# Performance work log

Hardware: AMD Instinct MI355X
Metric: run time of the kernel (lower is better)

The kernel has to match this reference:

```python
import jax, jax.numpy as jnp
import numpy as np

B, N, D = 2, 2048, 2048
H, KVH, HD = 16, 4, 128
GROUPS = H // KVH
MAG = 0.5
GATE_NORM = 16.0


def setup_inputs() -> dict:
    key = jax.random.key(0)
    ks = jax.random.split(key, 5)
    s = 0.02
    return {
        "hidden_states": jax.random.normal(ks[0], (B, N, D), jnp.float32),
        "wq": jax.random.normal(ks[1], (D, H * HD), jnp.float32) * s,
        "wk": jax.random.normal(ks[2], (D, KVH * HD), jnp.float32) * s,
        "wv": jax.random.normal(ks[3], (D, KVH * HD), jnp.float32) * s,
        "wo": jax.random.normal(ks[4], (H * HD, D), jnp.float32) * s,
    }


def _split_heads(x, h):
    # [b, n, h*d] -> [b, h, n, d]
    b, n, _ = x.shape
    return x.reshape(b, n, h, -1).transpose(0, 2, 1, 3)


def _repeat_kv(x, g):
    # [b, kvh, n, d] -> [b, kvh*g, n, d]
    return jnp.repeat(x, g, axis=1)


def _delta_rule(q, k, v, g):
    """Gated delta-rule linear attention (sequential scan == chunked result).
    q,k,v,g: [b,h,n,d]; returns o: [b,h,n,d], final state S: [b,h,d,d]."""
    beta = jnp.exp(g)  # g = logsigmoid(.)/16 -> beta = sigmoid(.)^{1/16} in (0,1)
    S0 = jnp.zeros(q.shape[:2] + (q.shape[-1], v.shape[-1]), q.dtype)

    def step(S, inp):
        qt, kt, vt, bt = inp  # each [b,h,d]
        pred = jnp.einsum("bhd,bhde->bhe", kt, S)
        S = S + jnp.einsum("bhd,bhe->bhde", kt * bt, vt - pred)
        ot = jnp.einsum("bhd,bhde->bhe", qt, S)
        return S, ot

    tl = lambda x: jnp.moveaxis(x, 2, 0)  # time-leading
    S, o = jax.lax.scan(step, S0, (tl(q), tl(k), tl(v), tl(beta)))
    return jnp.moveaxis(o, 0, 2), S


def reference(hidden_states, wq, wk, wv, wo):
    q = hidden_states @ wq          # [b,n,H*HD]
    k = hidden_states @ wk          # [b,n,KVH*HD]
    v = hidden_states @ wv
    g = k                           # AdaptiveAvgPool1d(out=KVH*HD) on k of width KVH*HD == identity

    qh = _split_heads(q, H)                         # [b,H,n,hd]
    kh = _repeat_kv(_split_heads(k, KVH), GROUPS)   # [b,H,n,hd]
    vh = _repeat_kv(_split_heads(v, KVH), GROUPS)
    gh = _repeat_kv(_split_heads(g, KVH), GROUPS)

    # --- linear (delta-rule) branch ---
    ql = jax.nn.softmax(qh, axis=-1)
    kl = jax.nn.softmax(kh, axis=-1)
    gl = jax.nn.log_sigmoid(gh) / GATE_NORM
    o_lin, _state = _delta_rule(ql, kl, vh, gl)
    o_lin = o_lin.transpose(0, 2, 1, 3).reshape(B, N, H * HD) @ wo

    # --- base causal softmax attention branch (same projections, same o_proj) ---
    scores = jnp.einsum("bhnd,bhmd->bhnm", qh, kh) / np.sqrt(HD).astype(np.float32)
    causal = jnp.tril(jnp.ones((N, N), bool))
    scores = jnp.where(causal[None, None], scores, jnp.float32(-1e30))
    probs = jax.nn.softmax(scores, axis=-1)
    o_base = jnp.einsum("bhnm,bhmd->bhnd", probs, vh)
    o_base = o_base.transpose(0, 2, 1, 3).reshape(B, N, H * HD) @ wo

    return MAG * o_lin + (1.0 - MAG) * o_base
```

## Files before the change

### kernel.cpp

```cpp
#include <hip/hip_runtime.h>


typedef unsigned short u16;
typedef short bf16x8 __attribute__((ext_vector_type(8)));
typedef float f32x4 __attribute__((ext_vector_type(4)));

#define DEV static __device__ __forceinline__

DEV f32x4 mfma(bf16x8 a, bf16x8 b, f32x4 c) {
  return __builtin_amdgcn_mfma_f32_16x16x32_bf16(a, b, c, 0, 0, 0);
}
DEV u16 f2b(float f) {
  unsigned int u = __builtin_bit_cast(unsigned int, f);
  u = (u + 0x7FFF + ((u >> 16) & 1)) >> 16;
  return (u16)u;
}
DEV float b2f(u16 b) {
  unsigned int u = ((unsigned int)b) << 16;
  return __builtin_bit_cast(float, u);
}
DEV float logsig(float x) { return fminf(x, 0.f) - log1pf(__expf(-fabsf(x))); }

DEV void gll16(const u16* g, u16* l) {
  __builtin_amdgcn_global_load_lds(
      (const __attribute__((address_space(1))) void*)g,
      (__attribute__((address_space(3))) void*)l, 16, 0, 0);
}

__global__ __launch_bounds__(256) void k_prep0(const float* __restrict__ hs,
    const float* __restrict__ wq, const float* __restrict__ wk,
    const float* __restrict__ wv, const float* __restrict__ wo,
    u16* __restrict__ hsb, u16* __restrict__ wqkvT, u16* __restrict__ woT) {
  int bid = blockIdx.x;
  int t = threadIdx.x;
  if (bid < 2048) {
    for (int it = 0; it < 4; it++) {
      long i = (long)bid * 4096 + it * 1024 + t * 4;
      const float4 v = *(const float4*)&hs[i];
      u16 o[4] = {f2b(v.x), f2b(v.y), f2b(v.z), f2b(v.w)};
      *(uint2*)&hsb[i] = *(const uint2*)o;
    }
    return;
  }
  bid -= 2048;
  __shared__ u16 T[64][72];
  const float* s; int sLD; long c0; u16* d; int nb, kb;
  if (bid < 1536) {
    int tn = bid >> 5, tk = bid & 31;
    nb = tn * 64; kb = tk * 64; d = wqkvT;
    if (nb < 2048)      { s = wq; sLD = 2048; c0 = nb; }
    else if (nb < 2560) { s = wk; sLD = 512;  c0 = nb - 2048; }
    else                { s = wv; sLD = 512;  c0 = nb - 2560; }
  } else {
    int b2 = bid - 1536;
    int tn = b2 >> 5, tk = b2 & 31;
    nb = tn * 64; kb = tk * 64; d = woT; s = wo; sLD = 2048; c0 = nb;
  }
  int lr = t >> 4, lc = (t & 15) * 4;
  for (int it = 0; it < 4; it++) {
    int r = lr + it * 16;
    float4 v = *(const float4*)&s[(long)(kb + r) * sLD + c0 + lc];
    u16 o[4] = {f2b(v.x), f2b(v.y), f2b(v.z), f2b(v.w)};
    *(uint2*)&T[r][lc] = *(const uint2*)o;
  }
  __syncthreads();
  int nl = t >> 2, kc = (t & 3) * 16;
  u16 pk[16];
  for (int i = 0; i < 16; i++) pk[i] = T[kc + i][nl];
  u16* dp = &d[(long)(nb + nl) * 2048 + kb + kc];
  *(uint4*)dp = *(const uint4*)pk;
  *(uint4*)(dp + 8) = *(const uint4*)(pk + 8);
}

template <int OUT_F32>
__global__ __launch_bounds__(256) void k_gemm(const u16* __restrict__ A,
    const u16* __restrict__ Bt, void* __restrict__ Cout, int M, int N, int K) {
  __shared__ u16 As[8192];
  __shared__ u16 Bs[8192];
  int t = threadIdx.x;
  int w = t >> 6, ln = t & 63, l15 = ln & 15, q = ln >> 4;
  long rb = (long)blockIdx.y * 128, cb = (long)blockIdx.x * 128;
  int wm = (w >> 1) * 64, wn = (w & 1) * 64;
  f32x4 acc[4][4] = {};
  int sr = t >> 3, sc = (t & 7) << 3;
  const u16* Ag = &A[(rb + sr) * (long)K + sc];
  const u16* Bg = &Bt[(cb + sr) * (long)K + sc];
  u16* Asl = &As[t * 8];
  u16* Bsl = &Bs[t * 8];
  for (int k0 = 0; k0 < K; k0 += 64) {
    __syncthreads();
    for (int it = 0; it < 4; it++) {
      gll16(Ag + (long)it * 32 * K + k0, Asl + it * 2048);
      gll16(Bg + (long)it * 32 * K + k0, Bsl + it * 2048);
    }
    __syncthreads();
    for (int ks = 0; ks < 2; ks++) {
      bf16x8 af[4], bfr[4];
      for (int mt = 0; mt < 4; mt++)
        af[mt] = *(const bf16x8*)&As[(wm + mt * 16 + l15) * 64 + ks * 32 + q * 8];
      for (int nt = 0; nt < 4; nt++)
        bfr[nt] = *(const bf16x8*)&Bs[(wn + nt * 16 + l15) * 64 + ks * 32 + q * 8];
      for (int mt = 0; mt < 4; mt++)
        for (int nt = 0; nt < 4; nt++)
          acc[mt][nt] = mfma(af[mt], bfr[nt], acc[mt][nt]);
    }
  }
  for (int mt = 0; mt < 4; mt++)
    for (int nt = 0; nt < 4; nt++)
      for (int r = 0; r < 4; r++) {
        long m = rb + wm + mt * 16 + q * 4 + r;
        long n = cb + wn + nt * 16 + l15;
        if (OUT_F32) ((float*)Cout)[m * N + n] = acc[mt][nt][r];
        else ((u16*)Cout)[m * N + n] = f2b(acc[mt][nt][r]);
      }
}

__global__ __launch_bounds__(256) void k_softq(const u16* __restrict__ qkv,
                                               u16* __restrict__ qsb) {
  int job = blockIdx.x * 4 + (threadIdx.x >> 6);
  int ln = threadIdx.x & 63;
  long row = job >> 4; int h = job & 15;
  const u16* src = &qkv[row * 3072 + h * 128];
  float x0 = b2f(src[ln * 2]), x1 = b2f(src[ln * 2 + 1]);
  float mx = fmaxf(x0, x1);
  for (int off = 1; off < 64; off <<= 1) mx = fmaxf(mx, __shfl_xor(mx, off));
  float e0 = __expf(x0 - mx), e1 = __expf(x1 - mx);
  float sm = e0 + e1;
  for (int off = 1; off < 64; off <<= 1) sm += __shfl_xor(sm, off);
  float inv = 1.f / sm;
  u16* dst = &qsb[row * 2048 + h * 128];
  dst[ln * 2] = f2b(e0 * inv);
  dst[ln * 2 + 1] = f2b(e1 * inv);
}

__global__ __launch_bounds__(256) void k_prepkv(const u16* __restrict__ qkv,
    u16* __restrict__ ksb, u16* __restrict__ kbb) {
  int job = blockIdx.x * 4 + (threadIdx.x >> 6);
  int ln = threadIdx.x & 63;
  long row = job >> 2; int kv = job & 3;
  const u16* srck = &qkv[row * 3072 + 2048 + kv * 128];
  float k0 = b2f(srck[ln * 2]), k1 = b2f(srck[ln * 2 + 1]);
  float mx = fmaxf(k0, k1);
  for (int off = 1; off < 64; off <<= 1) mx = fmaxf(mx, __shfl_xor(mx, off));
  float e0 = __expf(k0 - mx), e1 = __expf(k1 - mx);
  float sm = e0 + e1;
  for (int off = 1; off < 64; off <<= 1) sm += __shfl_xor(sm, off);
  float inv = 1.f / sm;
  float s0 = e0 * inv, s1 = e1 * inv;
  float bt0 = __expf(logsig(k0) * 0.0625f);
  float bt1 = __expf(logsig(k1) * 0.0625f);
  long o = row * 512 + kv * 128 + ln * 2;
  ksb[o] = f2b(s0); ksb[o + 1] = f2b(s1);
  kbb[o] = f2b(s0 * bt0); kbb[o + 1] = f2b(s1 * bt1);
}

__global__ __launch_bounds__(256) void k_transKV(const u16* __restrict__ kbb,
    const u16* __restrict__ qkv, u16* __restrict__ kbT, u16* __restrict__ vTb) {
  int bid = blockIdx.x;
  int nbk = bid & 31, db = ((bid >> 5) & 1) * 64, c8 = (bid >> 6) & 7, job = bid >> 9;
  int b = c8 >> 2, kv = c8 & 3;
  int nb = nbk * 64;
  __shared__ u16 T[64][72];
  int t = threadIdx.x;
  int nl = t >> 2, dc = (t & 3) * 16;
  const u16* src; long sLD, soff;
  if (job == 0) { src = kbb; sLD = 512;  soff = kv * 128; }
  else          { src = qkv; sLD = 3072; soff = 2560 + kv * 128; }
  const u16* sp = &src[((long)(b * 2048 + nb + nl)) * sLD + soff + db + dc];
  *(uint4*)&T[nl][dc] = *(const uint4*)sp;
  *(uint4*)&T[nl][dc + 8] = *(const uint4*)(sp + 8);
  __syncthreads();
  int dl = t >> 2, nc = (t & 3) * 16;
  u16 pk[16];
  for (int i = 0; i < 16; i++) pk[i] = T[nc + i][dl];
  u16* d = (job == 0) ? kbT : vTb;
  u16* dp = &d[((long)(c8 * 128 + db + dl)) * 2048 + nb + nc];
  *(uint4*)dp = *(const uint4*)pk;
  *(uint4*)(dp + 8) = *(const uint4*)(pk + 8);
}

__global__ __launch_bounds__(256) void k_phase1(const u16* __restrict__ ksb,
    const u16* __restrict__ kbb, const u16* __restrict__ kbT,
    const u16* __restrict__ qkv, u16* __restrict__ W_g, u16* __restrict__ U0T_g,
    u16* __restrict__ M_g, float* __restrict__ NT_g) {
  __shared__ u16 Pm[64][72];
  __shared__ u16 PT[64][72];
  __shared__ u16 slab[4][64][72];
  int cc = blockIdx.x;
  int c8 = cc >> 5, j = cc & 31;
  int b = c8 >> 2, kv = c8 & 3;
  long rb = (long)b * 2048 + j * 64;
  int w = threadIdx.x >> 6, ln = threadIdx.x & 63, l15 = ln & 15, q = ln >> 4;
  {
    f32x4 a4[4] = {};
    int m0 = w * 16;
    for (int ks = 0; ks < 4; ks++) {
      bf16x8 af = *(const bf16x8*)&ksb[(rb + m0 + l15) * 512 + kv * 128 + ks * 32 + q * 8];
      for (int nt = 0; nt < 4; nt++) {
        bf16x8 bfr = *(const bf16x8*)&kbb[(rb + nt * 16 + l15) * 512 + kv * 128 + ks * 32 + q * 8];
        a4[nt] = mfma(af, bfr, a4[nt]);
      }
    }
    for (int nt = 0; nt < 4; nt++)
      for (int r = 0; r < 4; r++) {
        int m = m0 + q * 4 + r, n = nt * 16 + l15;
        u16 h = f2b((m > n) ? -a4[nt][r] : 0.f);
        Pm[m][n] = h; PT[n][m] = h;
      }
  }
  for (int idx = threadIdx.x; idx < 16384; idx += 256) {
    int s = idx >> 12, rem = idx & 4095, t = rem >> 6, c = rem & 63;
    u16 v;
    if (s < 2) v = ksb[(rb + t) * 512 + kv * 128 + s * 64 + c];
    else       v = qkv[(rb + t) * 3072 + 2560 + kv * 128 + (s - 2) * 64 + c];
    slab[s][c][t] = v;
  }
  __syncthreads();
  f32x4 X[4][4];
  for (int mt = 0; mt < 4; mt++)
    for (int nt = 0; nt < 4; nt++)
      for (int r = 0; r < 4; r++)
        X[mt][nt][r] = b2f(slab[w][nt * 16 + l15][mt * 16 + q * 4 + r]);
  for (int f = 0; f < 6; f++) {
    for (int ks = 0; ks < 2; ks++) {
      bf16x8 af[4], bfr[4];
      for (int mt = 0; mt < 4; mt++)
        af[mt] = *(const bf16x8*)&Pm[mt * 16 + l15][ks * 32 + q * 8];
      for (int nt = 0; nt < 4; nt++)
        bfr[nt] = *(const bf16x8*)&slab[w][nt * 16 + l15][ks * 32 + q * 8];
      for (int mt = 0; mt < 4; mt++)
        for (int nt = 0; nt < 4; nt++)
          X[mt][nt] = mfma(af[mt], bfr[nt], X[mt][nt]);
    }
    f32x4 pn[4] = {};
    if (f < 5) {
      int m0 = w * 16;
      for (int ks = 0; ks < 2; ks++) {
        bf16x8 af = *(const bf16x8*)&Pm[m0 + l15][ks * 32 + q * 8];
        for (int nt = 0; nt < 4; nt++) {
          bf16x8 bfr = *(const bf16x8*)&PT[nt * 16 + l15][ks * 32 + q * 8];
          pn[nt] = mfma(af, bfr, pn[nt]);
        }
      }
    }
    __syncthreads();
    for (int mt = 0; mt < 4; mt++)
      for (int nt = 0; nt < 4; nt++)
        for (int r = 0; r < 4; r++)
          slab[w][nt * 16 + l15][mt * 16 + q * 4 + r] = f2b(X[mt][nt][r]);
    if (f < 5) {
      int m0 = w * 16;
      for (int nt = 0; nt < 4; nt++)
        for (int r = 0; r < 4; r++) {
          int m = m0 + q * 4 + r, n = nt * 16 + l15;
          u16 h = f2b(pn[nt][r]);
          Pm[m][n] = h; PT[n][m] = h;
        }
    }
    __syncthreads();
  }
  for (int idx = threadIdx.x; idx < 8192; idx += 256) {
    int t = idx >> 7, d = idx & 127;
    W_g[(long)cc * 8192 + idx] = slab[d >> 6][d & 63][t];
  }
  for (int idx = threadIdx.x; idx < 8192; idx += 256) {
    int e = idx >> 6, t = idx & 63;
    U0T_g[(long)cc * 8192 + idx] = slab[2 + (e >> 6)][e & 63][t];
  }
  {
    f32x4 acc[2][8] = {};
    int m0 = w * 32;
    for (int ks = 0; ks < 2; ks++) {
      bf16x8 af[2], bfr[8];
      for (int mt = 0; mt < 2; mt++)
        af[mt] = *(const bf16x8*)&kbT[((long)(c8 * 128 + m0 + mt * 16 + l15)) * 2048 + j * 64 + ks * 32 + q * 8];
      for (int nt = 0; nt < 8; nt++) {
        int n = nt * 16 + l15;
        bfr[nt] = *(const bf16x8*)&slab[n >> 6][n & 63][ks * 32 + q * 8];
      }
      for (int mt = 0; mt < 2; mt++)
        for (int nt = 0; nt < 8; nt++)
          acc[mt][nt] = mfma(af[mt], bfr[nt], acc[mt][nt]);
    }
    for (int mt = 0; mt < 2; mt++)
      for (int nt = 0; nt < 8; nt++)
        for (int r = 0; r < 4; r++) {
          int i_ = m0 + mt * 16 + q * 4 + r, jj = nt * 16 + l15;
          M_g[(long)cc * 16384 + (long)i_ * 128 + jj] =
              f2b(((i_ == jj) ? 1.f : 0.f) - acc[mt][nt][r]);
        }
  }
  {
    f32x4 acc[2][8] = {};
    int m0 = w * 32;
    for (int ks = 0; ks < 2; ks++) {
      bf16x8 af[2], bfr[8];
      for (int mt = 0; mt < 2; mt++) {
        int e = m0 + mt * 16 + l15;
        af[mt] = *(const bf16x8*)&slab[2 + (e >> 6)][e & 63][ks * 32 + q * 8];
      }
      for (int nt = 0; nt < 8; nt++)
        bfr[nt] = *(const bf16x8*)&kbT[((long)(c8 * 128 + nt * 16 + l15)) * 2048 + j * 64 + ks * 32 + q * 8];
      for (int mt = 0; mt < 2; mt++)
        for (int nt = 0; nt < 8; nt++)
          acc[mt][nt] = mfma(af[mt], bfr[nt], acc[mt][nt]);
    }
    for (int mt = 0; mt < 2; mt++)
      for (int nt = 0; nt < 8; nt++)
        for (int r = 0; r < 4; r++) {
          int e = m0 + mt * 16 + q * 4 + r, i_ = nt * 16 + l15;
          NT_g[(long)cc * 16384 + (long)e * 128 + i_] = acc[mt][nt][r];
        }
  }
}

__global__ __launch_bounds__(256) void k_phase2(const u16* __restrict__ W_g,
    const u16* __restrict__ U0T_g, const u16* __restrict__ M_g,
    const float* __restrict__ NT_g, u16* __restrict__ St0_g,
    u16* __restrict__ UT_g) {
  __shared__ u16 St[16][136];
  int c8 = blockIdx.x & 7, eb = blockIdx.x >> 3;
  int e0 = eb * 16;
  int w = threadIdx.x >> 6, ln = threadIdx.x & 63, l15 = ln & 15, q = ln >> 4;
  for (int idx = threadIdx.x; idx < 16 * 128; idx += 256)
    St[idx >> 7][idx & 127] = 0;
  __syncthreads();
  for (int j = 0; j < 32; j++) {
    long cc = c8 * 32 + j;
    for (int idx = threadIdx.x; idx < 2048; idx += 256) {
      int e = idx >> 7, d = idx & 127;
      St0_g[cc * 16384 + (long)(e0 + e) * 128 + d] = St[e][d];
    }
    {
      f32x4 acc = {};
      for (int ks = 0; ks < 4; ks++) {
        bf16x8 af = *(const bf16x8*)&St[l15][ks * 32 + q * 8];
        bf16x8 bfr = *(const bf16x8*)&W_g[cc * 8192 + (long)(w * 16 + l15) * 128 + ks * 32 + q * 8];
        acc = mfma(af, bfr, acc);
      }
      for (int r = 0; r < 4; r++) {
        int e = q * 4 + r, t = w * 16 + l15;
        float v = b2f(U0T_g[cc * 8192 + (long)(e0 + e) * 64 + t]) - acc[r];
        UT_g[cc * 8192 + (long)(e0 + e) * 64 + t] = f2b(v);
      }
    }
    f32x4 acc2[2] = {};
    for (int ks = 0; ks < 4; ks++) {
      bf16x8 af = *(const bf16x8*)&St[l15][ks * 32 + q * 8];
      for (int nt = 0; nt < 2; nt++) {
        bf16x8 bfr = *(const bf16x8*)&M_g[cc * 16384 + (long)(w * 32 + nt * 16 + l15) * 128 + ks * 32 + q * 8];
        acc2[nt] = mfma(af, bfr, acc2[nt]);
      }
    }
    for (int nt = 0; nt < 2; nt++)
      for (int r = 0; r < 4; r++)
        acc2[nt][r] += NT_g[cc * 16384 + (long)(e0 + q * 4 + r) * 128 + w * 32 + nt * 16 + l15];
    __syncthreads();
    for (int nt = 0; nt < 2; nt++)
      for (int r = 0; r < 4; r++)
        St[q * 4 + r][w * 32 + nt * 16 + l15] = f2b(acc2[nt][r]);
    __syncthreads();
  }
}

__global__ __launch_bounds__(256) void k_phase3(const u16* __restrict__ qsb,
    const u16* __restrict__ kbb, const u16* __restrict__ St0_g,
    const u16* __restrict__ UT_g, u16* __restrict__ o_lin) {
  __shared__ u16 Pl[64][72];
  int cc = blockIdx.x >> 2, hh = blockIdx.x & 3;
  int c8 = cc >> 5, j = cc & 31;
  int b = c8 >> 2, kv = c8 & 3, hq = kv * 4 + hh;
  long rb = (long)b * 2048 + j * 64;
  int w = threadIdx.x >> 6, ln = threadIdx.x & 63, l15 = ln & 15, q = ln >> 4;
  int m0 = w * 16;
  f32x4 O[8] = {};
  for (int ks = 0; ks < 4; ks++) {
    bf16x8 af = *(const bf16x8*)&qsb[(rb + m0 + l15) * 2048 + hq * 128 + ks * 32 + q * 8];
    for (int nt = 0; nt < 8; nt++) {
      bf16x8 bfr = *(const bf16x8*)&St0_g[(long)cc * 16384 + (long)(nt * 16 + l15) * 128 + ks * 32 + q * 8];
      O[nt] = mfma(af, bfr, O[nt]);
    }
  }
  {
    f32x4 p4[4] = {};
    for (int ks = 0; ks < 4; ks++) {
      bf16x8 af = *(const bf16x8*)&qsb[(rb + m0 + l15) * 2048 + hq * 128 + ks * 32 + q * 8];
      for (int nt = 0; nt < 4; nt++) {
        bf16x8 bfr = *(const bf16x8*)&kbb[(rb + nt * 16 + l15) * 512 + kv * 128 + ks * 32 + q * 8];
        p4[nt] = mfma(af, bfr, p4[nt]);
      }
    }
    for (int nt = 0; nt < 4; nt++)
      for (int r = 0; r < 4; r++) {
        int m = m0 + q * 4 + r, n = nt * 16 + l15;
        Pl[m][n] = f2b((m >= n) ? p4[nt][r] : 0.f);
      }
  }
  __syncthreads();
  for (int ks = 0; ks < 2; ks++) {
    bf16x8 af = *(const bf16x8*)&Pl[m0 + l15][ks * 32 + q * 8];
    for (int nt = 0; nt < 8; nt++) {
      bf16x8 bfr = *(const bf16x8*)&UT_g[(long)cc * 8192 + (long)(nt * 16 + l15) * 64 + ks * 32 + q * 8];
      O[nt] = mfma(af, bfr, O[nt]);
    }
  }
  for (int nt = 0; nt < 8; nt++)
    for (int r = 0; r < 4; r++) {
      int m = m0 + q * 4 + r, e = nt * 16 + l15;
      o_lin[(rb + m) * 2048 + hq * 128 + e] = f2b(O[nt][r]);
    }
}

__global__ __launch_bounds__(256) void k_flash(const u16* __restrict__ qkv,
    const u16* __restrict__ vTb, const u16* __restrict__ o_lin,
    u16* __restrict__ o_comb) {
  __shared__ u16 P[2][32][136];
  __shared__ float psL[4][32];
  int pr = blockIdx.x & 31, h = (blockIdx.x >> 5) & 15, b = blockIdx.x >> 9;
  int kv = h >> 2;
  int w = threadIdx.x >> 6, ln = threadIdx.x & 63, l15 = ln & 15, q = ln >> 4;
  const float sc2 = 0.127517444f;
  const u16* vb_ = &vTb[((long)(b * 4 + kv) * 128 + w * 32) * 2048];
  long kvb = (long)b * 2048;
  for (int sel = 0; sel < 2; sel++) {
    int qt = sel ? 63 - pr : pr;
    long qb = kvb + qt * 32;
    int njt = (qt >> 2) + 1;
    bf16x8 bq[2][4];
    for (int nt = 0; nt < 2; nt++)
      for (int ks = 0; ks < 4; ks++)
        bq[nt][ks] = *(const bf16x8*)&qkv[(qb + nt * 16 + l15) * 3072 + h * 128 + ks * 32 + q * 8];
    f32x4 O[2][2] = {};
    float psum[2] = {0.f, 0.f};
    for (int jt = 0; jt < njt; jt++) {
      int buf = jt & 1;
      long kb = kvb + jt * 128;
      f32x4 st[2][2] = {};
      for (int ks = 0; ks < 4; ks++) {
        bf16x8 ak0 = *(const bf16x8*)&qkv[(kb + w * 32 + l15) * 3072 + 2048 + kv * 128 + ks * 32 + q * 8];
        bf16x8 ak1 = *(const bf16x8*)&qkv[(kb + w * 32 + 16 + l15) * 3072 + 2048 + kv * 128 + ks * 32 + q * 8];
        for (int nt = 0; nt < 2; nt++) {
          st[0][nt] = mfma(ak0, bq[nt][ks], st[0][nt]);
          st[1][nt] = mfma(ak1, bq[nt][ks], st[1][nt]);
        }
      }
      bool last = (jt == njt - 1);
      for (int mt = 0; mt < 2; mt++)
        for (int nt = 0; nt < 2; nt++) {
          int rg = qt * 32 + nt * 16 + l15;
          for (int r = 0; r < 4; r++) {
            int kg = jt * 128 + w * 32 + mt * 16 + q * 4 + r;
            float pv = exp2f(st[mt][nt][r] * sc2);
            if (last && kg > rg) pv = 0.f;
            st[mt][nt][r] = pv;
            psum[nt] += pv;
          }
        }
      for (int mt = 0; mt < 2; mt++)
        for (int nt = 0; nt < 2; nt++) {
          u16 pk[4];
          for (int r = 0; r < 4; r++) pk[r] = f2b(st[mt][nt][r]);
          *(uint2*)&P[buf][nt * 16 + l15][w * 32 + mt * 16 + q * 4] = *(const uint2*)pk;
        }
      __syncthreads();
      for (int ks = 0; ks < 4; ks++) {
        bf16x8 ap0 = *(const bf16x8*)&P[buf][l15][ks * 32 + q * 8];
        bf16x8 ap1 = *(const bf16x8*)&P[buf][16 + l15][ks * 32 + q * 8];
        bf16x8 bv0 = *(const bf16x8*)&vb_[(long)l15 * 2048 + jt * 128 + ks * 32 + q * 8];
        bf16x8 bv1 = *(const bf16x8*)&vb_[(long)(16 + l15) * 2048 + jt * 128 + ks * 32 + q * 8];
        O[0][0] = mfma(ap0, bv0, O[0][0]);
        O[0][1] = mfma(ap0, bv1, O[0][1]);
        O[1][0] = mfma(ap1, bv0, O[1][0]);
        O[1][1] = mfma(ap1, bv1, O[1][1]);
      }
    }
    for (int nt = 0; nt < 2; nt++) {
      float s = psum[nt];
      s += __shfl_xor(s, 16);
      s += __shfl_xor(s, 32);
      if (q == 0) psL[w][nt * 16 + l15] = s;
    }
    __syncthreads();
    for (int mtp = 0; mtp < 2; mtp++)
      for (int r = 0; r < 4; r++) {
        int row = mtp * 16 + q * 4 + r;
        float tot = psL[0][row] + psL[1][row] + psL[2][row] + psL[3][row];
        float linv = 1.f / tot;
        for (int ntv = 0; ntv < 2; ntv++) {
          long off = (qb + row) * 2048 + h * 128 + w * 32 + ntv * 16 + l15;
          o_comb[off] = f2b(0.5f * O[mtp][ntv][r] * linv + 0.5f * b2f(o_lin[off]));
        }
      }
    __syncthreads();
  }
}

extern "C" void kernel_launch(void* const* d_in, const int* in_sizes, int n_in,
                              void* d_out, int out_size, void* d_ws, size_t ws_size,
                              hipStream_t stream) {
  const float* hs = (const float*)d_in[0];
  const float* wq = (const float*)d_in[1];
  const float* wk = (const float*)d_in[2];
  const float* wv = (const float*)d_in[3];
  const float* wo = (const float*)d_in[4];

  char* p = (char*)d_ws;
  auto alloc = [&](size_t bytes) {
    char* r = p;
    p += (bytes + 255) & ~(size_t)255;
    return r;
  };
  u16* hsb    = (u16*)alloc(16777216);
  u16* wqkvT  = (u16*)alloc(12582912);
  u16* woT    = (u16*)alloc(8388608);
  u16* qkv    = (u16*)alloc(25165824);
  u16* qsb    = (u16*)alloc(16777216);
  u16* ksb    = (u16*)alloc(4194304);
  u16* kbb    = (u16*)alloc(4194304);
  u16* kbT    = (u16*)alloc(4194304);
  u16* vTb    = (u16*)alloc(4194304);
  u16* o_lin  = (u16*)alloc(16777216);
  u16* W_g    = (u16*)alloc(4194304);
  u16* U0T_g  = (u16*)alloc(4194304);
  u16* M_g    = (u16*)alloc(8388608);
  float* NT_g = (float*)alloc(16777216);
  u16* St0_g  = (u16*)alloc(8388608);
  u16* UT_g   = (u16*)alloc(4194304);

  k_prep0<<<4608, 256, 0, stream>>>(hs, wq, wk, wv, wo, hsb, wqkvT, woT);
  k_gemm<0><<<dim3(24, 32), 256, 0, stream>>>(hsb, wqkvT, qkv, 4096, 3072, 2048);
  k_softq<<<16384, 256, 0, stream>>>(qkv, qsb);
  k_prepkv<<<4096, 256, 0, stream>>>(qkv, ksb, kbb);
  k_transKV<<<1024, 256, 0, stream>>>(kbb, qkv, kbT, vTb);
  k_phase1<<<256, 256, 0, stream>>>(ksb, kbb, kbT, qkv, W_g, U0T_g, M_g, NT_g);
  k_phase2<<<64, 256, 0, stream>>>(W_g, U0T_g, M_g, NT_g, St0_g, UT_g);
  k_phase3<<<1024, 256, 0, stream>>>(qsb, kbb, St0_g, UT_g, o_lin);
  k_flash<<<1024, 256, 0, stream>>>(qkv, vTb, o_lin, hsb);
  k_gemm<1><<<dim3(16, 32), 256, 0, stream>>>(hsb, woT, (float*)d_out, 4096, 2048, 2048);
}
```

Measured before the change: 580.8 us.

## Fuse activation kernels, pipeline phase2 loads, restructure flash attention tiling

Three elementwise and transpose kernels (q softmax, k softmax with gate, K/V transpose) become one vectorized kernel with packed bf16 stores, cutting launches and memory passes. Phase1 writes U0 and NT transposed so phase2 can double-buffer its per-chunk operand loads in registers and overlap them with the serial state recurrence. Flash attention switches to 16-row query tiles, 2048 blocks and a launch-bounds occupancy hint. Each wave now holds its own key slice with no per-tile block barrier and prefetches the next K tile, then combines partial outputs in shared memory. The new bf16 pack truncates ties differently from the old round-to-nearest-even conversion.

```diff
diff --git a/kernel.cpp b/kernel.cpp
--- a/kernel.cpp
+++ b/kernel.cpp
@@ -18,6 +18,11 @@
 DEV float b2f(u16 b) {
   unsigned int u = ((unsigned int)b) << 16;
   return __builtin_bit_cast(float, u);
+}
+DEV unsigned packbf(float a, float b) {
+  unsigned ua = __builtin_bit_cast(unsigned, a) + 0x8000u;
+  unsigned ub = __builtin_bit_cast(unsigned, b) + 0x8000u;
+  return (ua >> 16) | (ub & 0xffff0000u);
 }
 DEV float logsig(float x) { return fminf(x, 0.f) - log1pf(__expf(-fabsf(x))); }
 
@@ -115,74 +120,111 @@
       }
 }
 
-__global__ __launch_bounds__(256) void k_softq(const u16* __restrict__ qkv,
-                                               u16* __restrict__ qsb) {
-  int job = blockIdx.x * 4 + (threadIdx.x >> 6);
-  int ln = threadIdx.x & 63;
-  long row = job >> 4; int h = job & 15;
-  const u16* src = &qkv[row * 3072 + h * 128];
-  float x0 = b2f(src[ln * 2]), x1 = b2f(src[ln * 2 + 1]);
-  float mx = fmaxf(x0, x1);
-  for (int off = 1; off < 64; off <<= 1) mx = fmaxf(mx, __shfl_xor(mx, off));
-  float e0 = __expf(x0 - mx), e1 = __expf(x1 - mx);
-  float sm = e0 + e1;
-  for (int off = 1; off < 64; off <<= 1) sm += __shfl_xor(sm, off);
-  float inv = 1.f / sm;
-  u16* dst = &qsb[row * 2048 + h * 128];
-  dst[ln * 2] = f2b(e0 * inv);
-  dst[ln * 2 + 1] = f2b(e1 * inv);
-}
-
-__global__ __launch_bounds__(256) void k_prepkv(const u16* __restrict__ qkv,
-    u16* __restrict__ ksb, u16* __restrict__ kbb) {
-  int job = blockIdx.x * 4 + (threadIdx.x >> 6);
-  int ln = threadIdx.x & 63;
-  long row = job >> 2; int kv = job & 3;
-  const u16* srck = &qkv[row * 3072 + 2048 + kv * 128];
-  float k0 = b2f(srck[ln * 2]), k1 = b2f(srck[ln * 2 + 1]);
-  float mx = fmaxf(k0, k1);
-  for (int off = 1; off < 64; off <<= 1) mx = fmaxf(mx, __shfl_xor(mx, off));
-  float e0 = __expf(k0 - mx), e1 = __expf(k1 - mx);
-  float sm = e0 + e1;
-  for (int off = 1; off < 64; off <<= 1) sm += __shfl_xor(sm, off);
-  float inv = 1.f / sm;
-  float s0 = e0 * inv, s1 = e1 * inv;
-  float bt0 = __expf(logsig(k0) * 0.0625f);
-  float bt1 = __expf(logsig(k1) * 0.0625f);
-  long o = row * 512 + kv * 128 + ln * 2;
-  ksb[o] = f2b(s0); ksb[o + 1] = f2b(s1);
-  kbb[o] = f2b(s0 * bt0); kbb[o + 1] = f2b(s1 * bt1);
-}
-
-__global__ __launch_bounds__(256) void k_transKV(const u16* __restrict__ kbb,
-    const u16* __restrict__ qkv, u16* __restrict__ kbT, u16* __restrict__ vTb) {
-  int bid = blockIdx.x;
-  int nbk = bid & 31, db = ((bid >> 5) & 1) * 64, c8 = (bid >> 6) & 7, job = bid >> 9;
-  int b = c8 >> 2, kv = c8 & 3;
-  int nb = nbk * 64;
-  __shared__ u16 T[64][72];
-  int t = threadIdx.x;
-  int nl = t >> 2, dc = (t & 3) * 16;
-  const u16* src; long sLD, soff;
-  if (job == 0) { src = kbb; sLD = 512;  soff = kv * 128; }
-  else          { src = qkv; sLD = 3072; soff = 2560 + kv * 128; }
-  const u16* sp = &src[((long)(b * 2048 + nb + nl)) * sLD + soff + db + dc];
-  *(uint4*)&T[nl][dc] = *(const uint4*)sp;
-  *(uint4*)&T[nl][dc + 8] = *(const uint4*)(sp + 8);
+__global__ __launch_bounds__(256) void k_act(const u16* __restrict__ qkv,
+    u16* __restrict__ qsb, u16* __restrict__ ksb, u16* __restrict__ kbb,
+    u16* __restrict__ kbT, u16* __restrict__ vTb) {
+  __shared__ u16 T[128][72];
+  int bid = blockIdx.x, t = threadIdx.x;
+  const float L2E = 1.442695041f;
+  if (bid < 1024) {
+    int h = bid & 15;
+    long rb = (long)(bid >> 4) * 64;
+    int row = t >> 2, c = (t & 3) * 32;
+    const u16* src = &qkv[(rb + row) * 3072 + h * 128 + c];
+    float x[32];
+    for (int i = 0; i < 4; i++) {
+      uint4 v = *(const uint4*)&src[i * 8];
+      unsigned vv[4] = {v.x, v.y, v.z, v.w};
+      for (int jj = 0; jj < 4; jj++) {
+        x[i * 8 + jj * 2] = b2f((u16)(vv[jj] & 0xffff));
+        x[i * 8 + jj * 2 + 1] = b2f((u16)(vv[jj] >> 16));
+      }
+    }
+    float mx = x[0];
+    for (int i = 1; i < 32; i++) mx = fmaxf(mx, x[i]);
+    mx = fmaxf(mx, __shfl_xor(mx, 1));
+    mx = fmaxf(mx, __shfl_xor(mx, 2));
+    float sm = 0.f;
+    for (int i = 0; i < 32; i++) { x[i] = exp2f((x[i] - mx) * L2E); sm += x[i]; }
+    sm += __shfl_xor(sm, 1);
+    sm += __shfl_xor(sm, 2);
+    float inv = 1.f / sm;
+    unsigned pk[16];
+    for (int i = 0; i < 16; i++) pk[i] = packbf(x[2 * i] * inv, x[2 * i + 1] * inv);
+    u16* dst = &qsb[(rb + row) * 2048 + h * 128 + c];
+    for (int i = 0; i < 4; i++) *(uint4*)&dst[i * 8] = *(const uint4*)&pk[i * 4];
+    return;
+  }
+  int idx = bid - 1024;
+  int isV = idx >= 256;
+  if (isV) idx -= 256;
+  int kvg = idx & 3;
+  long rb = (long)(idx >> 2) * 64;
+  int row = t >> 2, c = (t & 3) * 32;
+  int b = (int)(rb >> 11);
+  int c8 = b * 4 + kvg;
+  long nloc = rb & 2047;
+  if (!isV) {
+    const u16* src = &qkv[(rb + row) * 3072 + 2048 + kvg * 128 + c];
+    float x[32];
+    for (int i = 0; i < 4; i++) {
+      uint4 v = *(const uint4*)&src[i * 8];
+      unsigned vv[4] = {v.x, v.y, v.z, v.w};
+      for (int jj = 0; jj < 4; jj++) {
+        x[i * 8 + jj * 2] = b2f((u16)(vv[jj] & 0xffff));
+        x[i * 8 + jj * 2 + 1] = b2f((u16)(vv[jj] >> 16));
+      }
+    }
+    float bt[32];
+    for (int i = 0; i < 32; i++) bt[i] = exp2f(logsig(x[i]) * 0.0901684411f);
+    float mx = x[0];
+    for (int i = 1; i < 32; i++) mx = fmaxf(mx, x[i]);
+    mx = fmaxf(mx, __shfl_xor(mx, 1));
+    mx = fmaxf(mx, __shfl_xor(mx, 2));
+    float sm = 0.f;
+    for (int i = 0; i < 32; i++) { x[i] = exp2f((x[i] - mx) * L2E); sm += x[i]; }
+    sm += __shfl_xor(sm, 1);
+    sm += __shfl_xor(sm, 2);
+    float inv = 1.f / sm;
+    unsigned pks[16], pkb[16];
+    for (int i = 0; i < 16; i++) {
+      float s0 = x[2 * i] * inv, s1 = x[2 * i + 1] * inv;
+      pks[i] = packbf(s0, s1);
+      pkb[i] = packbf(s0 * bt[2 * i], s1 * bt[2 * i + 1]);
+    }
+    u16* d1 = &ksb[(rb + row) * 512 + kvg * 128 + c];
+    u16* d2 = &kbb[(rb + row) * 512 + kvg * 128 + c];
+    for (int i = 0; i < 4; i++) {
+      *(uint4*)&d1[i * 8] = *(const uint4*)&pks[i * 4];
+      *(uint4*)&d2[i * 8] = *(const uint4*)&pkb[i * 4];
+    }
+    for (int i = 0; i < 16; i++) {
+      T[c + 2 * i][row] = (u16)(pkb[i] & 0xffff);
+      T[c + 2 * i + 1][row] = (u16)(pkb[i] >> 16);
+    }
+  } else {
+    const u16* src = &qkv[(rb + row) * 3072 + 2560 + kvg * 128 + c];
+    for (int i = 0; i < 4; i++) {
+      uint4 v = *(const uint4*)&src[i * 8];
+      unsigned vv[4] = {v.x, v.y, v.z, v.w};
+      for (int jj = 0; jj < 4; jj++) {
+        T[c + i * 8 + jj * 2][row] = (u16)(vv[jj] & 0xffff);
+        T[c + i * 8 + jj * 2 + 1][row] = (u16)(vv[jj] >> 16);
+      }
+    }
+  }
   __syncthreads();
-  int dl = t >> 2, nc = (t & 3) * 16;
-  u16 pk[16];
-  for (int i = 0; i < 16; i++) pk[i] = T[nc + i][dl];
-  u16* d = (job == 0) ? kbT : vTb;
-  u16* dp = &d[((long)(c8 * 128 + db + dl)) * 2048 + nb + nc];
-  *(uint4*)dp = *(const uint4*)pk;
-  *(uint4*)(dp + 8) = *(const uint4*)(pk + 8);
+  int dr = t >> 1, nc = (t & 1) * 32;
+  u16* dst = isV ? vTb : kbT;
+  u16* dp = &dst[((long)(c8 * 128 + dr)) * 2048 + nloc + nc];
+  for (int i = 0; i < 4; i++)
+    *(uint4*)&dp[i * 8] = *(const uint4*)&T[dr][nc + i * 8];
 }
 
 __global__ __launch_bounds__(256) void k_phase1(const u16* __restrict__ ksb,
     const u16* __restrict__ kbb, const u16* __restrict__ kbT,
-    const u16* __restrict__ qkv, u16* __restrict__ W_g, u16* __restrict__ U0T_g,
-    u16* __restrict__ M_g, float* __restrict__ NT_g) {
+    const u16* __restrict__ qkv, u16* __restrict__ W_g, u16* __restrict__ U0_g,
+    u16* __restrict__ M_g, float* __restrict__ NTT_g) {
   __shared__ u16 Pm[64][72];
   __shared__ u16 PT[64][72];
   __shared__ u16 slab[4][64][72];
@@ -264,8 +306,8 @@
     W_g[(long)cc * 8192 + idx] = slab[d >> 6][d & 63][t];
   }
   for (int idx = threadIdx.x; idx < 8192; idx += 256) {
-    int e = idx >> 6, t = idx & 63;
-    U0T_g[(long)cc * 8192 + idx] = slab[2 + (e >> 6)][e & 63][t];
+    int t = idx >> 7, e = idx & 127;
+    U0_g[(long)cc * 8192 + idx] = slab[2 + (e >> 6)][e & 63][t];
   }
   {
     f32x4 acc[2][8] = {};
@@ -295,12 +337,12 @@
     int m0 = w * 32;
     for (int ks = 0; ks < 2; ks++) {
       bf16x8 af[2], bfr[8];
-      for (int mt = 0; mt < 2; mt++) {
-        int e = m0 + mt * 16 + l15;
-        af[mt] = *(const bf16x8*)&slab[2 + (e >> 6)][e & 63][ks * 32 + q * 8];
-      }
-      for (int nt = 0; nt < 8; nt++)
-        bfr[nt] = *(const bf16x8*)&kbT[((long)(c8 * 128 + nt * 16 + l15)) * 2048 + j * 64 + ks * 32 + q * 8];
+      for (int mt = 0; mt < 2; mt++)
+        af[mt] = *(const bf16x8*)&kbT[((long)(c8 * 128 + m0 + mt * 16 + l15)) * 2048 + j * 64 + ks * 32 + q * 8];
+      for (int nt = 0; nt < 8; nt++) {
+        int e = nt * 16 + l15;
+        bfr[nt] = *(const bf16x8*)&slab[2 + (e >> 6)][e & 63][ks * 32 + q * 8];
+      }
       for (int mt = 0; mt < 2; mt++)
         for (int nt = 0; nt < 8; nt++)
           acc[mt][nt] = mfma(af[mt], bfr[nt], acc[mt][nt]);
@@ -308,15 +350,17 @@
     for (int mt = 0; mt < 2; mt++)
       for (int nt = 0; nt < 8; nt++)
         for (int r = 0; r < 4; r++) {
-          int e = m0 + mt * 16 + q * 4 + r, i_ = nt * 16 + l15;
-          NT_g[(long)cc * 16384 + (long)e * 128 + i_] = acc[mt][nt][r];
+          int i_ = m0 + mt * 16 + q * 4 + r, e = nt * 16 + l15;
+          NTT_g[(long)cc * 16384 + (long)i_ * 128 + e] = acc[mt][nt][r];
         }
   }
 }
 
+struct P2Buf { bf16x8 W[4]; bf16x8 M[4][2]; f32x4 NT[2]; ushort4 U0; };
+
 __global__ __launch_bounds__(256) void k_phase2(const u16* __restrict__ W_g,
-    const u16* __restrict__ U0T_g, const u16* __restrict__ M_g,
-    const float* __restrict__ NT_g, u16* __restrict__ St0_g,
+    const u16* __restrict__ U0_g, const u16* __restrict__ M_g,
+    const float* __restrict__ NTT_g, u16* __restrict__ St0_g,
     u16* __restrict__ UT_g) {
   __shared__ u16 St[16][136];
   int c8 = blockIdx.x & 7, eb = blockIdx.x >> 3;
@@ -325,41 +369,47 @@
   for (int idx = threadIdx.x; idx < 16 * 128; idx += 256)
     St[idx >> 7][idx & 127] = 0;
   __syncthreads();
-  for (int j = 0; j < 32; j++) {
-    long cc = c8 * 32 + j;
-    for (int idx = threadIdx.x; idx < 2048; idx += 256) {
-      int e = idx >> 7, d = idx & 127;
-      St0_g[cc * 16384 + (long)(e0 + e) * 128 + d] = St[e][d];
-    }
-    {
-      f32x4 acc = {};
-      for (int ks = 0; ks < 4; ks++) {
-        bf16x8 af = *(const bf16x8*)&St[l15][ks * 32 + q * 8];
-        bf16x8 bfr = *(const bf16x8*)&W_g[cc * 8192 + (long)(w * 16 + l15) * 128 + ks * 32 + q * 8];
-        acc = mfma(af, bfr, acc);
-      }
-      for (int r = 0; r < 4; r++) {
-        int e = q * 4 + r, t = w * 16 + l15;
-        float v = b2f(U0T_g[cc * 8192 + (long)(e0 + e) * 64 + t]) - acc[r];
-        UT_g[cc * 8192 + (long)(e0 + e) * 64 + t] = f2b(v);
-      }
-    }
-    f32x4 acc2[2] = {};
-    for (int ks = 0; ks < 4; ks++) {
-      bf16x8 af = *(const bf16x8*)&St[l15][ks * 32 + q * 8];
-      for (int nt = 0; nt < 2; nt++) {
-        bf16x8 bfr = *(const bf16x8*)&M_g[cc * 16384 + (long)(w * 32 + nt * 16 + l15) * 128 + ks * 32 + q * 8];
-        acc2[nt] = mfma(af, bfr, acc2[nt]);
-      }
-    }
+
+  auto loadbuf = [&](P2Buf& B, long cc) {
+    for (int ks = 0; ks < 4; ks++)
+      B.W[ks] = *(const bf16x8*)&W_g[cc * 8192 + (long)(w * 16 + l15) * 128 + ks * 32 + q * 8];
+    for (int ks = 0; ks < 4; ks++)
+      for (int nt = 0; nt < 2; nt++)
+        B.M[ks][nt] = *(const bf16x8*)&M_g[cc * 16384 + (long)(w * 32 + nt * 16 + l15) * 128 + ks * 32 + q * 8];
     for (int nt = 0; nt < 2; nt++)
-      for (int r = 0; r < 4; r++)
-        acc2[nt][r] += NT_g[cc * 16384 + (long)(e0 + q * 4 + r) * 128 + w * 32 + nt * 16 + l15];
+      B.NT[nt] = *(const f32x4*)&NTT_g[cc * 16384 + (long)(w * 32 + nt * 16 + l15) * 128 + e0 + q * 4];
+    B.U0 = *(const ushort4*)&U0_g[cc * 8192 + (long)(w * 16 + l15) * 128 + e0 + q * 4];
+  };
+
+  auto step = [&](long cc, P2Buf& cur, P2Buf& nxt, bool pf) {
+    if (pf) loadbuf(nxt, cc + 1);
+    for (int idx = threadIdx.x; idx < 2048; idx += 256)
+      St0_g[cc * 16384 + (long)(e0 + (idx >> 7)) * 128 + (idx & 127)] = St[idx >> 7][idx & 127];
+    bf16x8 sf[4];
+    for (int ks = 0; ks < 4; ks++)
+      sf[ks] = *(const bf16x8*)&St[l15][ks * 32 + q * 8];
+    f32x4 acc = {};
+    for (int ks = 0; ks < 4; ks++) acc = mfma(sf[ks], cur.W[ks], acc);
+    const u16* u0p = (const u16*)&cur.U0;
+    for (int r = 0; r < 4; r++)
+      UT_g[cc * 8192 + (long)(e0 + q * 4 + r) * 64 + w * 16 + l15] = f2b(b2f(u0p[r]) - acc[r]);
+    f32x4 acc2[2] = {cur.NT[0], cur.NT[1]};
+    for (int ks = 0; ks < 4; ks++)
+      for (int nt = 0; nt < 2; nt++)
+        acc2[nt] = mfma(sf[ks], cur.M[ks][nt], acc2[nt]);
     __syncthreads();
     for (int nt = 0; nt < 2; nt++)
       for (int r = 0; r < 4; r++)
         St[q * 4 + r][w * 32 + nt * 16 + l15] = f2b(acc2[nt][r]);
     __syncthreads();
+  };
+
+  P2Buf A, B;
+  long base = (long)c8 * 32;
+  loadbuf(A, base);
+  for (int j = 0; j < 32; j += 2) {
+    step(base + j, A, B, true);
+    step(base + j + 1, B, A, j + 2 < 32);
   }
 }
 
@@ -411,86 +461,100 @@
     }
 }
 
-__global__ __launch_bounds__(256) void k_flash(const u16* __restrict__ qkv,
+__global__ __launch_bounds__(256, 2) void k_flash(const u16* __restrict__ qkv,
     const u16* __restrict__ vTb, const u16* __restrict__ o_lin,
     u16* __restrict__ o_comb) {
-  __shared__ u16 P[2][32][136];
-  __shared__ float psL[4][32];
-  int pr = blockIdx.x & 31, h = (blockIdx.x >> 5) & 15, b = blockIdx.x >> 9;
+  __shared__ u16 P[4][16][40];
+  __shared__ float Ored[2][128][20];
+  __shared__ float psL[4][16];
+  int pr = blockIdx.x & 63, h = (blockIdx.x >> 6) & 15, b = blockIdx.x >> 10;
   int kv = h >> 2;
   int w = threadIdx.x >> 6, ln = threadIdx.x & 63, l15 = ln & 15, q = ln >> 4;
   const float sc2 = 0.127517444f;
-  const u16* vb_ = &vTb[((long)(b * 4 + kv) * 128 + w * 32) * 2048];
+  u16 (*Pw)[40] = P[w];
+  const u16* kbase = &qkv[2048 + kv * 128];
+  const u16* vbase = &vTb[(long)(b * 4 + kv) * 128 * 2048 + w * 32];
   long kvb = (long)b * 2048;
   for (int sel = 0; sel < 2; sel++) {
-    int qt = sel ? 63 - pr : pr;
-    long qb = kvb + qt * 32;
-    int njt = (qt >> 2) + 1;
-    bf16x8 bq[2][4];
-    for (int nt = 0; nt < 2; nt++)
+    int qt = sel ? 127 - pr : pr;
+    long qb = kvb + qt * 16;
+    int njt = (qt >> 3) + 1;
+    bf16x8 bq[4];
+    for (int ks = 0; ks < 4; ks++)
+      bq[ks] = *(const bf16x8*)&qkv[(qb + l15) * 3072 + h * 128 + ks * 32 + q * 8];
+    f32x4 O[8] = {};
+    float psum = 0.f;
+    bf16x8 akA[2][4], akB[2][4];
+    for (int mt = 0; mt < 2; mt++)
       for (int ks = 0; ks < 4; ks++)
-        bq[nt][ks] = *(const bf16x8*)&qkv[(qb + nt * 16 + l15) * 3072 + h * 128 + ks * 32 + q * 8];
-    f32x4 O[2][2] = {};
-    float psum[2] = {0.f, 0.f};
-    for (int jt = 0; jt < njt; jt++) {
-      int buf = jt & 1;
-      long kb = kvb + jt * 128;
-      f32x4 st[2][2] = {};
-      for (int ks = 0; ks < 4; ks++) {
-        bf16x8 ak0 = *(const bf16x8*)&qkv[(kb + w * 32 + l15) * 3072 + 2048 + kv * 128 + ks * 32 + q * 8];
-        bf16x8 ak1 = *(const bf16x8*)&qkv[(kb + w * 32 + 16 + l15) * 3072 + 2048 + kv * 128 + ks * 32 + q * 8];
-        for (int nt = 0; nt < 2; nt++) {
-          st[0][nt] = mfma(ak0, bq[nt][ks], st[0][nt]);
-          st[1][nt] = mfma(ak1, bq[nt][ks], st[1][nt]);
+        akA[mt][ks] = *(const bf16x8*)&kbase[(kvb + w * 32 + mt * 16 + l15) * 3072 + ks * 32 + q * 8];
+
+    auto body = [&](int jt, bf16x8 (*cur)[4], bf16x8 (*nxt)[4]) {
+      if (jt + 1 < njt) {
+        long kb = kvb + (jt + 1) * 128;
+        for (int mt = 0; mt < 2; mt++)
+          for (int ks = 0; ks < 4; ks++)
+            nxt[mt][ks] = *(const bf16x8*)&kbase[(kb + w * 32 + mt * 16 + l15) * 3072 + ks * 32 + q * 8];
+      }
+      bf16x8 bv[8];
+      for (int et = 0; et < 8; et++)
+        bv[et] = *(const bf16x8*)&vbase[(long)(et * 16 + l15) * 2048 + jt * 128 + q * 8];
+      f32x4 st[2] = {};
+      for (int ks = 0; ks < 4; ks++)
+        for (int mt = 0; mt < 2; mt++)
+          st[mt] = mfma(cur[mt][ks], bq[ks], st[mt]);
+      bool last = (jt == njt - 1);
+      int rg = qt * 16 + l15;
+      for (int mt = 0; mt < 2; mt++) {
+        for (int r = 0; r < 4; r++) {
+          float pv = exp2f(st[mt][r] * sc2);
+          int kg = jt * 128 + w * 32 + mt * 16 + q * 4 + r;
+          if (last && kg > rg) pv = 0.f;
+          st[mt][r] = pv;
+          psum += pv;
         }
-      }
-      bool last = (jt == njt - 1);
-      for (int mt = 0; mt < 2; mt++)
-        for (int nt = 0; nt < 2; nt++) {
-          int rg = qt * 32 + nt * 16 + l15;
-          for (int r = 0; r < 4; r++) {
-            int kg = jt * 128 + w * 32 + mt * 16 + q * 4 + r;
-            float pv = exp2f(st[mt][nt][r] * sc2);
-            if (last && kg > rg) pv = 0.f;
-            st[mt][nt][r] = pv;
-            psum[nt] += pv;
-          }
-        }
-      for (int mt = 0; mt < 2; mt++)
-        for (int nt = 0; nt < 2; nt++) {
-          u16 pk[4];
-          for (int r = 0; r < 4; r++) pk[r] = f2b(st[mt][nt][r]);
-          *(uint2*)&P[buf][nt * 16 + l15][w * 32 + mt * 16 + q * 4] = *(const uint2*)pk;
-        }
-      __syncthreads();
-      for (int ks = 0; ks < 4; ks++) {
-        bf16x8 ap0 = *(const bf16x8*)&P[buf][l15][ks * 32 + q * 8];
-        bf16x8 ap1 = *(const bf16x8*)&P[buf][16 + l15][ks * 32 + q * 8];
-        bf16x8 bv0 = *(const bf16x8*)&vb_[(long)l15 * 2048 + jt * 128 + ks * 32 + q * 8];
-        bf16x8 bv1 = *(const bf16x8*)&vb_[(long)(16 + l15) * 2048 + jt * 128 + ks * 32 + q * 8];
-        O[0][0] = mfma(ap0, bv0, O[0][0]);
-        O[0][1] = mfma(ap0, bv1, O[0][1]);
-        O[1][0] = mfma(ap1, bv0, O[1][0]);
-        O[1][1] = mfma(ap1, bv1, O[1][1]);
-      }
-    }
-    for (int nt = 0; nt < 2; nt++) {
-      float s = psum[nt];
-      s += __shfl_xor(s, 16);
-      s += __shfl_xor(s, 32);
-      if (q == 0) psL[w][nt * 16 + l15] = s;
-    }
-    __syncthreads();
-    for (int mtp = 0; mtp < 2; mtp++)
-      for (int r = 0; r < 4; r++) {
-        int row = mtp * 16 + q * 4 + r;
+        unsigned pu[2];
+        pu[0] = packbf(st[mt][0], st[mt][1]);
+        pu[1] = packbf(st[mt][2], st[mt][3]);
+        *(uint2*)&Pw[l15][mt * 16 + q * 4] = *(const uint2*)pu;
+      }
+      bf16x8 ap = *(const bf16x8*)&Pw[l15][q * 8];
+      for (int et = 0; et < 8; et++)
+        O[et] = mfma(ap, bv[et], O[et]);
+    };
+    for (int jt = 0; jt < njt; jt += 2) {
+      body(jt, akA, akB);
+      if (jt + 1 < njt) body(jt + 1, akB, akA);
+    }
+    psum += __shfl_xor(psum, 16);
+    psum += __shfl_xor(psum, 32);
+    if (q == 0) psL[w][l15] = psum;
+    __syncthreads();
+    if (w < 2)
+      for (int et = 0; et < 8; et++)
+        *(f32x4*)&Ored[w][et * 16 + l15][q * 4] = O[et];
+    __syncthreads();
+    if (w >= 2)
+      for (int et = 0; et < 8; et++) {
+        f32x4 acc = *(const f32x4*)&Ored[w - 2][et * 16 + l15][q * 4];
+        acc += O[et];
+        *(f32x4*)&Ored[w - 2][et * 16 + l15][q * 4] = acc;
+      }
+    __syncthreads();
+    {
+      int e = threadIdx.x & 127, half = threadIdx.x >> 7;
+      f32x4 s0 = *(const f32x4*)&Ored[0][e][half * 8];
+      f32x4 s1 = *(const f32x4*)&Ored[0][e][half * 8 + 4];
+      s0 += *(const f32x4*)&Ored[1][e][half * 8];
+      s1 += *(const f32x4*)&Ored[1][e][half * 8 + 4];
+      for (int i = 0; i < 8; i++) {
+        int row = half * 8 + i;
         float tot = psL[0][row] + psL[1][row] + psL[2][row] + psL[3][row];
-        float linv = 1.f / tot;
-        for (int ntv = 0; ntv < 2; ntv++) {
-          long off = (qb + row) * 2048 + h * 128 + w * 32 + ntv * 16 + l15;
-          o_comb[off] = f2b(0.5f * O[mtp][ntv][r] * linv + 0.5f * b2f(o_lin[off]));
-        }
-      }
+        float val = (i < 4 ? s0[i] : s1[i - 4]) / tot;
+        long off = (qb + row) * 2048 + h * 128 + e;
+        o_comb[off] = f2b(0.5f * val + 0.5f * b2f(o_lin[off]));
+      }
+    }
     __syncthreads();
   }
 }
@@ -521,20 +585,18 @@
   u16* vTb    = (u16*)alloc(4194304);
   u16* o_lin  = (u16*)alloc(16777216);
   u16* W_g    = (u16*)alloc(4194304);
-  u16* U0T_g  = (u16*)alloc(4194304);
+  u16* U0_g   = (u16*)alloc(4194304);
   u16* M_g    = (u16*)alloc(8388608);
-  float* NT_g = (float*)alloc(16777216);
+  float* NTT_g = (float*)alloc(16777216);
   u16* St0_g  = (u16*)alloc(8388608);
   u16* UT_g   = (u16*)alloc(4194304);
 
   k_prep0<<<4608, 256, 0, stream>>>(hs, wq, wk, wv, wo, hsb, wqkvT, woT);
   k_gemm<0><<<dim3(24, 32), 256, 0, stream>>>(hsb, wqkvT, qkv, 4096, 3072, 2048);
-  k_softq<<<16384, 256, 0, stream>>>(qkv, qsb);
-  k_prepkv<<<4096, 256, 0, stream>>>(qkv, ksb, kbb);
-  k_transKV<<<1024, 256, 0, stream>>>(kbb, qkv, kbT, vTb);
-  k_phase1<<<256, 256, 0, stream>>>(ksb, kbb, kbT, qkv, W_g, U0T_g, M_g, NT_g);
-  k_phase2<<<64, 256, 0, stream>>>(W_g, U0T_g, M_g, NT_g, St0_g, UT_g);
+  k_act<<<1536, 256, 0, stream>>>(qkv, qsb, ksb, kbb, kbT, vTb);
+  k_phase1<<<256, 256, 0, stream>>>(ksb, kbb, kbT, qkv, W_g, U0_g, M_g, NTT_g);
+  k_phase2<<<64, 256, 0, stream>>>(W_g, U0_g, M_g, NTT_g, St0_g, UT_g);
   k_phase3<<<1024, 256, 0, stream>>>(qsb, kbb, St0_g, UT_g, o_lin);
-  k_flash<<<1024, 256, 0, stream>>>(qkv, vTb, o_lin, hsb);
+  k_flash<<<2048, 256, 0, stream>>>(qkv, vTb, o_lin, hsb);
   k_gemm<1><<<dim3(16, 32), 256, 0, stream>>>(hsb, woT, (float*)d_out, 4096, 2048, 2048);
 }
```

Measured after the change: 651.8 us. 1.12x slower.
